# Performance work log

Hardware: AMD Instinct MI355X
Metric: run time of the kernel (lower is better)

## Reference

```python
import jax, jax.numpy as jnp
import numpy as np

B, IN, H = 4096, 2048, 2048


def setup_inputs() -> dict:
    key = jax.random.key(0)
    ks = jax.random.split(key, 20)
    s_in = 1.0 / np.sqrt(IN)
    s_h = 1.0 / np.sqrt(H)
    inp = {
        "x": jax.random.normal(ks[0], (B, IN), jnp.float32),
        "h": jax.random.normal(ks[1], (B, H), jnp.float32),
        "c": jax.random.normal(ks[2], (B, H), jnp.float32),
    }
    names_in = [("Wii", "bii"), ("Wif", "bif"), ("Wig", "big"), ("Wio", "bio")]
    names_h = [("Whi", "bhi"), ("Whf", "bhf"), ("Whg", "bhg"), ("Who", "bho")]
    k = 3
    for wn, bn in names_in:
        inp[wn] = jax.random.normal(ks[k], (H, IN), jnp.float32) * s_in
        inp[bn] = jax.random.normal(ks[k + 1], (H,), jnp.float32) * s_in
        k += 2
    for wn, bn in names_h:
        inp[wn] = jax.random.normal(ks[k], (H, H), jnp.float32) * s_h
        inp[bn] = jax.random.normal(ks[k + 1], (H,), jnp.float32) * s_h
        k += 2
    return inp


def reference(x, h, c, Wii, bii, Whi, bhi, Wif, bif, Whf, bhf,
              Wig, big, Whg, bhg, Wio, bio, Who, bho):
    # Fuse the 4 input-projections and 4 hidden-projections into two GEMMs
    # (same math as 8 separate nn.Linear calls).
    Wx = jnp.concatenate([Wii, Wif, Wig, Wio], axis=0)   # [4H, IN]
    Wh = jnp.concatenate([Whi, Whf, Whg, Who], axis=0)   # [4H, H]
    bx = jnp.concatenate([bii, bif, big, bio])            # [4H]
    bh = jnp.concatenate([bhi, bhf, bhg, bho])            # [4H]
    gates = x @ Wx.T + h @ Wh.T + bx + bh                 # [B, 4H]
    ii, ff, gg, oo = jnp.split(gates, 4, axis=-1)
    i = jax.nn.sigmoid(ii)
    f = jax.nn.sigmoid(ff)
    g = jnp.tanh(gg)
    o = jax.nn.sigmoid(oo)
    c_new = f * c + i * g
    h_new = o * jnp.tanh(c_new)
    return jnp.stack([h_new, c_new])  # [2, B, H]
```

## Files before the change

### kernel.cpp

```cpp
#include <hip/hip_runtime.h>
#include <stdint.h>

typedef __attribute__((ext_vector_type(4))) float f32x4;
typedef __attribute__((ext_vector_type(8))) short bf16x8;

#define MFMA_BF16 __builtin_amdgcn_mfma_f32_16x16x32_bf16

__device__ __forceinline__ unsigned short f2bf(float f) {
  union { float f; uint32_t u; } a; a.f = f;
  uint32_t u = a.u;
  uint32_t r = (u + 0x7FFFu + ((u >> 16) & 1u)) >> 16;
  return (unsigned short)r;
}

__device__ __forceinline__ bf16x8 cvt8(const float4 v0, const float4 v1) {
  bf16x8 o;
  o[0] = (short)f2bf(v0.x); o[1] = (short)f2bf(v0.y);
  o[2] = (short)f2bf(v0.z); o[3] = (short)f2bf(v0.w);
  o[4] = (short)f2bf(v1.x); o[5] = (short)f2bf(v1.y);
  o[6] = (short)f2bf(v1.z); o[7] = (short)f2bf(v1.w);
  return o;
}

__global__ void pack_all_kernel(const float4* __restrict__ x, const float4* __restrict__ hh,
                                const float* __restrict__ Wii, const float* __restrict__ Wif,
                                const float* __restrict__ Wig, const float* __restrict__ Wio,
                                const float* __restrict__ Whi, const float* __restrict__ Whf,
                                const float* __restrict__ Whg, const float* __restrict__ Who,
                                bf16x8* __restrict__ A, bf16x8* __restrict__ Wp2) {
  const int total = 6291456;
  for (int q = blockIdx.x * blockDim.x + threadIdx.x; q < total; q += gridDim.x * blockDim.x) {
    if (q < 2097152) {
      int row = q >> 9, c8 = q & 511;
      const float4* src = (c8 < 256) ? &x[row * 512 + c8 * 2] : &hh[row * 512 + (c8 - 256) * 2];
      A[q] = cvt8(src[0], src[1]);
    } else {
      int wq = q - 2097152;
      int lane = wq & 63;
      int fi = (wq >> 6) & 7;
      int wn = (wq >> 9) & 3;
      int T = (wq >> 11) & 63;
      int bn = wq >> 17;
      int ni = fi >> 1, kk = fi & 1;
      int H = (bn << 6) | (wn << 4) | (lane & 15);
      int k = (T << 6) | (kk << 5) | ((lane >> 4) << 3);
      const float* src;
      int kloc = k;
      if (k < 2048) { src = (ni == 0) ? Wii : (ni == 1) ? Wif : (ni == 2) ? Wig : Wio; }
      else { src = (ni == 0) ? Whi : (ni == 1) ? Whf : (ni == 2) ? Whg : Who; kloc = k - 2048; }
      const float4 v0 = *(const float4*)&src[(size_t)H * 2048 + kloc];
      const float4 v1 = *(const float4*)&src[(size_t)H * 2048 + kloc + 4];
      Wp2[wq] = cvt8(v0, v1);
    }
  }
}

#define AS1 __attribute__((address_space(1)))
#define AS3 __attribute__((address_space(3)))
#define GLD(srcp, dstE)                                                         \
  __builtin_amdgcn_global_load_lds((const AS1 void*)(srcp),                     \
                                   (AS3 void*)(&smem[dstE]), 16, 0, 0)

#define STGA(kO_, dstB_)                                                        \
  _Pragma("unroll") for (int j = 0; j < 4; ++j)                                 \
    GLD(aS + (size_t)j * 32768 + (kO_), (dstB_) + w * 2048 + j * 512)

#define LDB(T_, B_)                                                             \
  {                                                                             \
    const ushort* bp_ = bFrag + (size_t)(T_) * 16384;                           \
    _Pragma("unroll") for (int f = 0; f < 8; ++f)                               \
      B_[f] = *(const bf16x8*)&bp_[f * 512];                                    \
  }

#define RDA(bufE_, MIBASE, AF_)                                                 \
  _Pragma("unroll") for (int m = 0; m < 4; ++m) {                               \
    AF_[m][0] = *(const bf16x8*)&smem[(bufE_) + aRb + ((MIBASE) + m) * 1024 + colE0]; \
    AF_[m][1] = *(const bf16x8*)&smem[(bufE_) + aRb + ((MIBASE) + m) * 1024 + colE1]; \
  }

#define Q32(AROW, AF_, B_)                                                      \
  __builtin_amdgcn_s_setprio(1);                                                \
  _Pragma("unroll") for (int m = 0; m < 4; ++m)                                 \
    _Pragma("unroll") for (int ni = 0; ni < 4; ++ni) {                          \
      acc[(AROW) + m][ni] = MFMA_BF16(AF_[m][0], B_[ni * 2], acc[(AROW) + m][ni], 0, 0, 0); \
      acc[(AROW) + m][ni] = MFMA_BF16(AF_[m][1], B_[ni * 2 + 1], acc[(AROW) + m][ni], 0, 0, 0); \
    }                                                                           \
  __builtin_amdgcn_s_setprio(0);

#define TILEX(T_, BUFE_, NBUFE_, BCUR, BNXT, LAST)                              \
  {                                                                             \
    if (!(LAST)) { STGA(((T_) + 1) << 6, NBUFE_); LDB((T_) + 1, BNXT); }        \
    bf16x8 af[4][2];                                                            \
    RDA(BUFE_, 0, af);                                                          \
    Q32(0, af, BCUR);                                                           \
    RDA(BUFE_, 4, af);                                                          \
    Q32(4, af, BCUR);                                                           \
    if (!(LAST)) {                                                              \
      asm volatile("s_waitcnt vmcnt(8)" ::: "memory");                          \
      __builtin_amdgcn_s_barrier();                                             \
    }                                                                           \
  }

__global__ __launch_bounds__(512, 2)
void lstm_gemm_kernel(const ushort* __restrict__ A, const ushort* __restrict__ Wp2,
                      const float* __restrict__ c,
                      const float* __restrict__ bii, const float* __restrict__ bif_,
                      const float* __restrict__ big_, const float* __restrict__ bio_,
                      const float* __restrict__ bhi, const float* __restrict__ bhf,
                      const float* __restrict__ bhg, const float* __restrict__ bho,
                      float* __restrict__ out) {
  __shared__ ushort smem[32768];
  const int tid = threadIdx.x;
  const int lane = tid & 63, w = tid >> 6;
  const int wm = w >> 2, wn = w & 3;

  const int bid = blockIdx.x;
  const int xcd = bid & 7, qq = bid >> 3;
  const int bn = (xcd << 2) | (qq >> 4);
  const int bm = qq & 15;

  const int laneRow = lane & 15, lane16 = lane >> 4;
  const int lr7 = laneRow & 7;
  const int colE0 = (lane16 ^ lr7) << 3;
  const int colE1 = ((4 + lane16) ^ lr7) << 3;
  const int aRb = (wm * 128 + laneRow) * 64;

  const int chunkOff = ((lane & 7) ^ (lane >> 3)) << 3;
  const ushort* aS = A + (size_t)(bm * 256 + 32 * w + (lane >> 3)) * 4096 + chunkOff;

  const ushort* bFrag = Wp2 + (size_t)bn * 64 * 16384 + wn * 4096 + lane * 8;

  f32x4 acc[8][4];
#pragma unroll
  for (int i = 0; i < 8; i++)
#pragma unroll
    for (int j = 0; j < 4; j++) acc[i][j] = (f32x4){0.f, 0.f, 0.f, 0.f};

  bf16x8 bA[8], bB[8];

  STGA(0, 0);
  LDB(0, bA);
  asm volatile("s_waitcnt vmcnt(8)" ::: "memory");
  __builtin_amdgcn_s_barrier();

#pragma unroll 1
  for (int T = 0; T < 62; T += 2) {
    TILEX(T, 0, 16384, bA, bB, false);
    TILEX(T + 1, 16384, 0, bB, bA, false);
  }
  TILEX(62, 0, 16384, bA, bB, false);
  TILEX(63, 16384, 0, bB, bA, true);

  const int hcol = bn * 64 + wn * 16 + laneRow;
  const float bI = bii[hcol] + bhi[hcol];
  const float bF = bif_[hcol] + bhf[hcol];
  const float bG = big_[hcol] + bhg[hcol];
  const float bO = bio_[hcol] + bho[hcol];
#pragma unroll
  for (int mi = 0; mi < 8; ++mi) {
    const int rowBase = bm * 256 + wm * 128 + mi * 16 + lane16 * 4;
#pragma unroll
    for (int rr = 0; rr < 4; ++rr) {
      const int row = rowBase + rr;
      const float ii = acc[mi][0][rr] + bI;
      const float ff = acc[mi][1][rr] + bF;
      const float gg = acc[mi][2][rr] + bG;
      const float oo = acc[mi][3][rr] + bO;
      const float iv = 1.f / (1.f + __expf(-ii));
      const float fv = 1.f / (1.f + __expf(-ff));
      const float gv = tanhf(gg);
      const float ov = 1.f / (1.f + __expf(-oo));
      const float cv = c[(size_t)row * 2048 + hcol];
      const float cn = fv * cv + iv * gv;
      const float hn = ov * tanhf(cn);
      out[(size_t)row * 2048 + hcol] = hn;
      out[(size_t)8388608 + (size_t)row * 2048 + hcol] = cn;
    }
  }
}

extern "C" void kernel_launch(void* const* d_in, const int* in_sizes, int n_in,
                              void* d_out, int out_size, void* d_ws, size_t ws_size,
                              hipStream_t stream) {
  const float* x = (const float*)d_in[0];
  const float* h = (const float*)d_in[1];
  const float* c = (const float*)d_in[2];
  const float* Wii = (const float*)d_in[3];  const float* bii = (const float*)d_in[4];
  const float* Wif = (const float*)d_in[5];  const float* bif_ = (const float*)d_in[6];
  const float* Wig = (const float*)d_in[7];  const float* big_ = (const float*)d_in[8];
  const float* Wio = (const float*)d_in[9];  const float* bio_ = (const float*)d_in[10];
  const float* Whi = (const float*)d_in[11]; const float* bhi = (const float*)d_in[12];
  const float* Whf = (const float*)d_in[13]; const float* bhf = (const float*)d_in[14];
  const float* Whg = (const float*)d_in[15]; const float* bhg = (const float*)d_in[16];
  const float* Who = (const float*)d_in[17]; const float* bho = (const float*)d_in[18];

  ushort* Abf = (ushort*)d_ws;
  ushort* Wpk = Abf + (size_t)4096 * 4096;
  float* out = (float*)d_out;

  pack_all_kernel<<<3072, 256, 0, stream>>>((const float4*)x, (const float4*)h,
                                            Wii, Wif, Wig, Wio, Whi, Whf, Whg, Who,
                                            (bf16x8*)Abf, (bf16x8*)Wpk);
  lstm_gemm_kernel<<<512, 512, 0, stream>>>(Abf, Wpk, c,
                                            bii, bif_, big_, bio_, bhi, bhf, bhg, bho, out);
}
```

Baseline: 323.9 us.

## Stage both A and B tiles through LDS with smaller 128x256 tiles

Weights are now packed row-major in bf16 and loaded into LDS with global_load_lds alongside A, replacing the per-wave direct register loads of pre-swizzled B fragments. The block tile shrinks from 256 rows to 128 rows with a K step of 32, doubling the grid to 1024 blocks and raising the occupancy target to 4 blocks per CU with smaller accumulators. The aim is more resident waves and shared B reuse across waves, at the cost of twice as many K iterations, each with a full vmcnt(0) wait and barrier, and so less latency hiding per step.

```diff
diff --git a/kernel.cpp b/kernel.cpp
--- a/kernel.cpp
+++ b/kernel.cpp
@@ -27,7 +27,7 @@
                                 const float* __restrict__ Wig, const float* __restrict__ Wio,
                                 const float* __restrict__ Whi, const float* __restrict__ Whf,
                                 const float* __restrict__ Whg, const float* __restrict__ Who,
-                                bf16x8* __restrict__ A, bf16x8* __restrict__ Wp2) {
+                                bf16x8* __restrict__ A, bf16x8* __restrict__ Wp) {
   const int total = 6291456;
   for (int q = blockIdx.x * blockDim.x + threadIdx.x; q < total; q += gridDim.x * blockDim.x) {
     if (q < 2097152) {
@@ -36,21 +36,20 @@
       A[q] = cvt8(src[0], src[1]);
     } else {
       int wq = q - 2097152;
-      int lane = wq & 63;
-      int fi = (wq >> 6) & 7;
-      int wn = (wq >> 9) & 3;
-      int T = (wq >> 11) & 63;
-      int bn = wq >> 17;
-      int ni = fi >> 1, kk = fi & 1;
-      int H = (bn << 6) | (wn << 4) | (lane & 15);
-      int k = (T << 6) | (kk << 5) | ((lane >> 4) << 3);
+      int p = wq >> 9, k8 = wq & 511;
+      int r = p & 255;
+      int g = (r >> 4) & 3;
+      int H = ((p >> 8) << 6) | ((r >> 6) << 4) | (r & 15);
       const float* src;
-      int kloc = k;
-      if (k < 2048) { src = (ni == 0) ? Wii : (ni == 1) ? Wif : (ni == 2) ? Wig : Wio; }
-      else { src = (ni == 0) ? Whi : (ni == 1) ? Whf : (ni == 2) ? Whg : Who; kloc = k - 2048; }
-      const float4 v0 = *(const float4*)&src[(size_t)H * 2048 + kloc];
-      const float4 v1 = *(const float4*)&src[(size_t)H * 2048 + kloc + 4];
-      Wp2[wq] = cvt8(v0, v1);
+      int k;
+      if (k8 < 256) {
+        src = (g == 0) ? Wii : (g == 1) ? Wif : (g == 2) ? Wig : Wio; k = k8 << 3;
+      } else {
+        src = (g == 0) ? Whi : (g == 1) ? Whf : (g == 2) ? Whg : Who; k = (k8 - 256) << 3;
+      }
+      const float4 v0 = *(const float4*)&src[(size_t)H * 2048 + k];
+      const float4 v1 = *(const float4*)&src[(size_t)H * 2048 + k + 4];
+      Wp[wq] = cvt8(v0, v1);
     }
   }
 }
@@ -61,95 +60,79 @@
   __builtin_amdgcn_global_load_lds((const AS1 void*)(srcp),                     \
                                    (AS3 void*)(&smem[dstE]), 16, 0, 0)
 
-#define STGA(kO_, dstB_)                                                        \
-  _Pragma("unroll") for (int j = 0; j < 4; ++j)                                 \
-    GLD(aS + (size_t)j * 32768 + (kO_), (dstB_) + w * 2048 + j * 512)
-
-#define LDB(T_, B_)                                                             \
+#define STAGE(T_, obuf_)                                                        \
   {                                                                             \
-    const ushort* bp_ = bFrag + (size_t)(T_) * 16384;                           \
-    _Pragma("unroll") for (int f = 0; f < 8; ++f)                               \
-      B_[f] = *(const bf16x8*)&bp_[f * 512];                                    \
+    const size_t kO_ = (size_t)(T_) * 32;                                       \
+    GLD(aS + kO_, (obuf_) + dA);                                                \
+    GLD(bS + kO_, (obuf_) + dB);                                                \
+    GLD(bS + (size_t)16 * 4096 + kO_, (obuf_) + dB + 512);                      \
   }
 
-#define RDA(bufE_, MIBASE, AF_)                                                 \
-  _Pragma("unroll") for (int m = 0; m < 4; ++m) {                               \
-    AF_[m][0] = *(const bf16x8*)&smem[(bufE_) + aRb + ((MIBASE) + m) * 1024 + colE0]; \
-    AF_[m][1] = *(const bf16x8*)&smem[(bufE_) + aRb + ((MIBASE) + m) * 1024 + colE1]; \
-  }
-
-#define Q32(AROW, AF_, B_)                                                      \
-  __builtin_amdgcn_s_setprio(1);                                                \
-  _Pragma("unroll") for (int m = 0; m < 4; ++m)                                 \
-    _Pragma("unroll") for (int ni = 0; ni < 4; ++ni) {                          \
-      acc[(AROW) + m][ni] = MFMA_BF16(AF_[m][0], B_[ni * 2], acc[(AROW) + m][ni], 0, 0, 0); \
-      acc[(AROW) + m][ni] = MFMA_BF16(AF_[m][1], B_[ni * 2 + 1], acc[(AROW) + m][ni], 0, 0, 0); \
-    }                                                                           \
-  __builtin_amdgcn_s_setprio(0);
-
-#define TILEX(T_, BUFE_, NBUFE_, BCUR, BNXT, LAST)                              \
+#define TILE(T_, buf_, obuf_, DOST_, SYNC_)                                     \
   {                                                                             \
-    if (!(LAST)) { STGA(((T_) + 1) << 6, NBUFE_); LDB((T_) + 1, BNXT); }        \
-    bf16x8 af[4][2];                                                            \
-    RDA(BUFE_, 0, af);                                                          \
-    Q32(0, af, BCUR);                                                           \
-    RDA(BUFE_, 4, af);                                                          \
-    Q32(4, af, BCUR);                                                           \
-    if (!(LAST)) {                                                              \
-      asm volatile("s_waitcnt vmcnt(8)" ::: "memory");                          \
+    if (DOST_) { STAGE((T_) + 1, obuf_); }                                      \
+    bf16x8 af[4], bf[4];                                                        \
+    _Pragma("unroll") for (int m = 0; m < 4; ++m)                               \
+      af[m] = *(const bf16x8*)&smem[(buf_) + aRb + m * 512 + colE];             \
+    _Pragma("unroll") for (int n = 0; n < 4; ++n)                               \
+      bf[n] = *(const bf16x8*)&smem[(buf_) + bRb + n * 512 + colE];             \
+    __builtin_amdgcn_s_setprio(1);                                              \
+    _Pragma("unroll") for (int m = 0; m < 4; ++m)                               \
+      _Pragma("unroll") for (int n = 0; n < 4; ++n)                             \
+        acc[m][n] = MFMA_BF16(af[m], bf[n], acc[m][n], 0, 0, 0);                \
+    __builtin_amdgcn_s_setprio(0);                                              \
+    if (SYNC_) {                                                                \
+      asm volatile("s_waitcnt vmcnt(0)" ::: "memory");                          \
       __builtin_amdgcn_s_barrier();                                             \
     }                                                                           \
   }
 
-__global__ __launch_bounds__(512, 2)
-void lstm_gemm_kernel(const ushort* __restrict__ A, const ushort* __restrict__ Wp2,
+__global__ __launch_bounds__(512, 4)
+void lstm_gemm_kernel(const ushort* __restrict__ A, const ushort* __restrict__ Wp,
                       const float* __restrict__ c,
                       const float* __restrict__ bii, const float* __restrict__ bif_,
                       const float* __restrict__ big_, const float* __restrict__ bio_,
                       const float* __restrict__ bhi, const float* __restrict__ bhf,
                       const float* __restrict__ bhg, const float* __restrict__ bho,
                       float* __restrict__ out) {
-  __shared__ ushort smem[32768];
+  __shared__ ushort smem[24576];
   const int tid = threadIdx.x;
   const int lane = tid & 63, w = tid >> 6;
   const int wm = w >> 2, wn = w & 3;
 
   const int bid = blockIdx.x;
   const int xcd = bid & 7, qq = bid >> 3;
-  const int bn = (xcd << 2) | (qq >> 4);
-  const int bm = qq & 15;
+  const int bn = (xcd << 2) | (qq >> 5);
+  const int bm = qq & 31;
 
   const int laneRow = lane & 15, lane16 = lane >> 4;
-  const int lr7 = laneRow & 7;
-  const int colE0 = (lane16 ^ lr7) << 3;
-  const int colE1 = ((4 + lane16) ^ lr7) << 3;
-  const int aRb = (wm * 128 + laneRow) * 64;
+  const int colE = ((lane16 ^ (laneRow & 3)) << 3);
+  const int aRb = (wm * 64 + laneRow) * 32;
+  const int bRb = 4096 + (wn * 64 + laneRow) * 32;
 
-  const int chunkOff = ((lane & 7) ^ (lane >> 3)) << 3;
-  const ushort* aS = A + (size_t)(bm * 256 + 32 * w + (lane >> 3)) * 4096 + chunkOff;
+  const int chunkOff = ((lane & 3) ^ ((lane >> 2) & 3)) << 3;
+  const ushort* aS = A + (size_t)(bm * 128 + 16 * w + (lane >> 2)) * 4096 + chunkOff;
+  const ushort* bS = Wp + (size_t)(bn * 256 + 32 * w + (lane >> 2)) * 4096 + chunkOff;
+  const int dA = w * 512;
+  const int dB = 4096 + w * 1024;
 
-  const ushort* bFrag = Wp2 + (size_t)bn * 64 * 16384 + wn * 4096 + lane * 8;
-
-  f32x4 acc[8][4];
+  f32x4 acc[4][4];
 #pragma unroll
-  for (int i = 0; i < 8; i++)
+  for (int i = 0; i < 4; i++)
 #pragma unroll
     for (int j = 0; j < 4; j++) acc[i][j] = (f32x4){0.f, 0.f, 0.f, 0.f};
 
-  bf16x8 bA[8], bB[8];
-
-  STGA(0, 0);
-  LDB(0, bA);
-  asm volatile("s_waitcnt vmcnt(8)" ::: "memory");
+  STAGE(0, 0);
+  asm volatile("s_waitcnt vmcnt(0)" ::: "memory");
   __builtin_amdgcn_s_barrier();
 
 #pragma unroll 1
-  for (int T = 0; T < 62; T += 2) {
-    TILEX(T, 0, 16384, bA, bB, false);
-    TILEX(T + 1, 16384, 0, bB, bA, false);
+  for (int T = 0; T < 126; T += 2) {
+    TILE(T, 0, 12288, true, true);
+    TILE(T + 1, 12288, 0, true, true);
   }
-  TILEX(62, 0, 16384, bA, bB, false);
-  TILEX(63, 16384, 0, bB, bA, true);
+  TILE(126, 0, 12288, true, true);
+  TILE(127, 12288, 0, false, false);
 
   const int hcol = bn * 64 + wn * 16 + laneRow;
   const float bI = bii[hcol] + bhi[hcol];
@@ -157,8 +140,8 @@
   const float bG = big_[hcol] + bhg[hcol];
   const float bO = bio_[hcol] + bho[hcol];
 #pragma unroll
-  for (int mi = 0; mi < 8; ++mi) {
-    const int rowBase = bm * 256 + wm * 128 + mi * 16 + lane16 * 4;
+  for (int mi = 0; mi < 4; ++mi) {
+    const int rowBase = bm * 128 + wm * 64 + mi * 16 + lane16 * 4;
 #pragma unroll
     for (int rr = 0; rr < 4; ++rr) {
       const int row = rowBase + rr;
@@ -201,6 +184,6 @@
   pack_all_kernel<<<3072, 256, 0, stream>>>((const float4*)x, (const float4*)h,
                                             Wii, Wif, Wig, Wio, Whi, Whf, Whg, Who,
                                             (bf16x8*)Abf, (bf16x8*)Wpk);
-  lstm_gemm_kernel<<<512, 512, 0, stream>>>(Abf, Wpk, c,
-                                            bii, bif_, big_, bio_, bhi, bhf, bhg, bho, out);
+  lstm_gemm_kernel<<<1024, 512, 0, stream>>>(Abf, Wpk, c,
+                                             bii, bif_, big_, bio_, bhi, bhf, bhg, bho, out);
 }
```

New measurement: 331.9 us. 2.5% more time.
